# Optimization experiments

Measured on AMD Instinct MI355X. Metric: run time of the kernel, lower is better.

## Reference

```python
import jax, jax.numpy as jnp
import numpy as np

N_NODES = 8192
D_FEAT = 128
R_BITS = 8      # rows per band
B_BANDS = 64    # number of LSH bands
D_THRESH = 0.25 # cosine-distance threshold from LSH(z, d=0.25, ...)


def setup_inputs() -> dict:
    key = jax.random.key(0)
    k1, k2, k3 = jax.random.split(key, 3)
    z = jax.random.normal(k1, (N_NODES, D_FEAT), dtype=jnp.float32)
    # random hyperplanes for signed-projection LSH: r*b = 512 planes
    H = jax.random.normal(k2, (D_FEAT, R_BITS * B_BANDS), dtype=jnp.float32)
    edge_index = jax.random.randint(k3, (2, N_NODES * 16), 0, N_NODES, dtype=jnp.int64)
    return {"z": z, "H": H, "edge_index": edge_index}


def reference(z, H, edge_index):
    # edge_index is unused by forward_all (kept for signature fidelity).
    N = z.shape[0]
    # --- hyperplane LSH signatures ---
    bits = (z @ H) > 0                              # [N, r*b] bool
    bits = bits.reshape(N, B_BANDS, R_BITS)         # [N, b, r]
    powers = (2 ** jnp.arange(R_BITS)).astype(jnp.int32)
    codes = jnp.sum(bits.astype(jnp.int32) * powers, axis=-1)  # [N, b] band hash codes

    # --- candidate pairs: collide in at least one band (OR over bands) ---
    def band_or(mask, c):  # c: [N] codes for one band
        return mask | (c[:, None] == c[None, :]), None
    collide, _ = jax.lax.scan(band_or, jnp.zeros((N, N), dtype=bool), codes.T)

    # --- exact cosine similarity on candidates ---
    zn = z / jnp.linalg.norm(z, axis=1, keepdims=True)
    S = zn @ zn.T                                   # [N, N] cosine similarity
    dist = 1.0 - S                                  # cosine distance

    eye = jnp.eye(N, dtype=bool)
    # pairs kept by LSH: colliding, within distance threshold, off-diagonal
    keep = collide & (dist < D_THRESH) & (~eye)
    # adjacency[v1, v2] = 1 - dist = cos_sim (sigmoid=True path); identity on diagonal
    A = jnp.where(keep, S, 0.0) + eye.astype(S.dtype)
    return A
```

## Files before the change

kernel.cpp:

```cpp
#include <hip/hip_runtime.h>
#include <hip/hip_bf16.h>

#define N_NODES 8192
#define D_FEAT 128

typedef __bf16 bf16x8 __attribute__((ext_vector_type(8)));
typedef float f32x4 __attribute__((ext_vector_type(4)));

__device__ __forceinline__ void lgkm_barrier() {
  asm volatile("s_waitcnt lgkmcnt(0)\n\ts_barrier" ::: "memory");
}
__device__ __forceinline__ void lgkm_fence() {
  asm volatile("s_waitcnt lgkmcnt(0)" ::: "memory");
}

__device__ __attribute__((noinline)) bool lsh_collide(
    const float* __restrict__ z, const float* __restrict__ H, int i, int j) {
  for (int b = 0; b < 64; ++b) {
    unsigned ci = 0, cj = 0;
    for (int bit = 0; bit < 8; ++bit) {
      int col = b * 8 + bit;
      float di = 0.f, dj = 0.f;
      for (int k = 0; k < D_FEAT; ++k) {
        float h = H[(size_t)k * 512 + col];
        di += z[(size_t)i * D_FEAT + k] * h;
        dj += z[(size_t)j * D_FEAT + k] * h;
      }
      if (di > 0.f) ci |= (1u << bit);
      if (cj > 0.f) cj |= 0;
      if (dj > 0.f) cj |= (1u << bit);
    }
    if (ci == cj) return true;
  }
  return false;
}

__device__ __forceinline__ unsigned pack_bf16x2(float x, float y) {
  __hip_bfloat16 bx = __float2bfloat16(x), by = __float2bfloat16(y);
  return (unsigned)(*(unsigned short*)&bx) |
         ((unsigned)(*(unsigned short*)&by) << 16);
}

__device__ __forceinline__ void stage_tile128(const float* __restrict__ z, int blk,
                                              unsigned short (*T)[128], int tid) {
  int row = tid >> 1, half = tid & 1;
  const float4* src = (const float4*)(z + (size_t)(blk * 128 + row) * D_FEAT + half * 64);
  float4 v[16];
#pragma unroll
  for (int c = 0; c < 16; ++c) v[c] = src[c];
  float ss = 0.f;
#pragma unroll
  for (int c = 0; c < 16; ++c)
    ss += v[c].x * v[c].x + v[c].y * v[c].y + v[c].z * v[c].z + v[c].w * v[c].w;
  ss += __shfl_xor(ss, 1);
  float inv = rsqrtf(ss);
#pragma unroll
  for (int c = 0; c < 8; ++c) {
    float4 a = v[2 * c], b = v[2 * c + 1];
    uint4 o;
    o.x = pack_bf16x2(a.x * inv, a.y * inv);
    o.y = pack_bf16x2(a.z * inv, a.w * inv);
    o.z = pack_bf16x2(b.x * inv, b.y * inv);
    o.w = pack_bf16x2(b.z * inv, b.w * inv);
    ((uint4*)&T[row][0])[(half * 8 + c) ^ (row & 15)] = o;
  }
}

__device__ __forceinline__ void stage_tile64(const float* __restrict__ z, int row0,
                                             unsigned short (*T)[128], int tid) {
  int row = tid >> 2, q = tid & 3;
  const float4* src = (const float4*)(z + (size_t)(row0 + row) * D_FEAT + q * 32);
  float4 v[8];
#pragma unroll
  for (int c = 0; c < 8; ++c) v[c] = src[c];
  float ss = 0.f;
#pragma unroll
  for (int c = 0; c < 8; ++c)
    ss += v[c].x * v[c].x + v[c].y * v[c].y + v[c].z * v[c].z + v[c].w * v[c].w;
  ss += __shfl_xor(ss, 1);
  ss += __shfl_xor(ss, 2);
  float inv = rsqrtf(ss);
#pragma unroll
  for (int c = 0; c < 4; ++c) {
    float4 a = v[2 * c], b = v[2 * c + 1];
    uint4 o;
    o.x = pack_bf16x2(a.x * inv, a.y * inv);
    o.y = pack_bf16x2(a.z * inv, a.w * inv);
    o.z = pack_bf16x2(b.x * inv, b.y * inv);
    o.w = pack_bf16x2(b.z * inv, b.w * inv);
    ((uint4*)&T[row][0])[(q * 4 + c) ^ (row & 15)] = o;
  }
}

__global__ __launch_bounds__(256, 3) void sim_kernel(const float* __restrict__ z,
                                                     const float* __restrict__ H,
                                                     float* __restrict__ out) {
  __shared__ __align__(16) unsigned char smem_raw[49152];
  unsigned short (*As)[128] = (unsigned short (*)[128])smem_raw;
  unsigned short (*Bs)[128] = (unsigned short (*)[128])(smem_raw + 16384);
  float* fS = (float*)smem_raw;

  int tid = threadIdx.x;
  int b = (int)blockIdx.x;
  int bn = b & 63;
  int bm0 = b >> 6;

  int wv = tid >> 6, lane = tid & 63;
  int wm = (wv >> 1) * 32, wn = (wv & 1) * 64;
  int m16 = lane & 15, g = lane >> 4;
  float* slab = fS + wv * 1024;

  stage_tile128(z, bn, Bs, tid);

  for (int t = 0; t < 16; ++t) {
    int bm = bm0 * 16 + t;

    lgkm_barrier();
    stage_tile64(z, bm * 64, As, tid);
    lgkm_barrier();

    f32x4 acc[2][4] = {};
#pragma unroll
    for (int kc = 0; kc < 4; ++kc) {
      bf16x8 fa[2], fb[4];
      int chunk = kc * 4 + g;
      int cs = (chunk ^ m16) * 8;
#pragma unroll
      for (int tt = 0; tt < 2; ++tt) fa[tt] = *(const bf16x8*)&As[wm + tt * 16 + m16][cs];
#pragma unroll
      for (int tt = 0; tt < 4; ++tt) fb[tt] = *(const bf16x8*)&Bs[wn + tt * 16 + m16][cs];
#pragma unroll
      for (int tm = 0; tm < 2; ++tm)
#pragma unroll
        for (int tn = 0; tn < 4; ++tn)
          acc[tm][tn] = __builtin_amdgcn_mfma_f32_16x16x32_bf16(fa[tm], fb[tn], acc[tm][tn], 0, 0, 0);
    }

    lgkm_barrier();

#pragma unroll
    for (int tm = 0; tm < 2; ++tm) {
#pragma unroll
      for (int tn = 0; tn < 4; ++tn) {
        int colq = tn * 16 + m16;
        int j = bn * 128 + wn + colq;
        f32x4 c = acc[tm][tn];
#pragma unroll
        for (int r = 0; r < 4; ++r) {
          int rs = g * 4 + r;
          int i = bm * 64 + wm + tm * 16 + rs;
          float s = c[r];
          float val = 0.0f;
          if (i == j) {
            val = 1.0f;
          } else if (s > 0.75f) {
            if (lsh_collide(z, H, i, j)) val = s;
          }
          slab[rs * 64 + (((colq >> 2) ^ rs) << 2) + (colq & 3)] = val;
        }
      }
      lgkm_fence();
#pragma unroll
      for (int it = 0; it < 4; ++it) {
        int rs = it * 4 + g;
        f32x4 v = *(const f32x4*)&slab[rs * 64 + ((m16 ^ rs) << 2)];
        int grow = bm * 64 + wm + tm * 16 + rs;
        *(f32x4*)&out[(size_t)grow * N_NODES + bn * 128 + wn + m16 * 4] = v;
      }
    }
  }
}

extern "C" void kernel_launch(void* const* d_in, const int* in_sizes, int n_in,
                              void* d_out, int out_size, void* d_ws, size_t ws_size,
                              hipStream_t stream) {
  const float* z = (const float*)d_in[0];
  const float* H = (const float*)d_in[1];
  float* out = (float*)d_out;
  (void)d_ws; (void)ws_size;

  sim_kernel<<<512, 256, 0, stream>>>(z, H, out);
}
```

Measured before the change: 281.1 us.

## Add dedicated store warps to overlap output writes with next tile compute

The block grows to 512 threads. Four waves compute the MFMA tile and write the results into a 32 KB shared buffer, and four separate waves store the previous tile's results to global memory while the next tile is being staged and computed. This removes the compute waves' serialized epilogue stores and the per-wave slab barrier. In exchange it uses 80 KB of shared memory and twice as many threads per block, which lowers occupancy. The single shared output buffer depends on barrier ordering to avoid overwrite races.

New measurement: 476.3 us. 1.69x slower.

```diff
diff --git a/kernel.cpp b/kernel.cpp
--- a/kernel.cpp
+++ b/kernel.cpp
@@ -9,9 +9,6 @@
 
 __device__ __forceinline__ void lgkm_barrier() {
   asm volatile("s_waitcnt lgkmcnt(0)\n\ts_barrier" ::: "memory");
-}
-__device__ __forceinline__ void lgkm_fence() {
-  asm volatile("s_waitcnt lgkmcnt(0)" ::: "memory");
 }
 
 __device__ __attribute__((noinline)) bool lsh_collide(
@@ -27,7 +24,6 @@
         dj += z[(size_t)j * D_FEAT + k] * h;
       }
       if (di > 0.f) ci |= (1u << bit);
-      if (cj > 0.f) cj |= 0;
       if (dj > 0.f) cj |= (1u << bit);
     }
     if (ci == cj) return true;
@@ -92,83 +88,97 @@
   }
 }
 
-__global__ __launch_bounds__(256, 3) void sim_kernel(const float* __restrict__ z,
+__device__ __forceinline__ void store_fs(float* __restrict__ out,
+                                         const float* __restrict__ fS,
+                                         int bm, int bn, int st) {
+#pragma unroll
+  for (int it = 0; it < 8; ++it) {
+    int slot = st + 256 * it;
+    int row = slot >> 5, chunk = slot & 31;
+    f32x4 v = *(const f32x4*)&fS[row * 128 + ((chunk ^ (row & 31)) << 2)];
+    *(f32x4*)&out[(size_t)(bm * 64 + row) * N_NODES + bn * 128 + chunk * 4] = v;
+  }
+}
+
+__global__ __launch_bounds__(512, 4) void sim_kernel(const float* __restrict__ z,
                                                      const float* __restrict__ H,
                                                      float* __restrict__ out) {
-  __shared__ __align__(16) unsigned char smem_raw[49152];
+  __shared__ __align__(16) unsigned char smem_raw[81920];
   unsigned short (*As)[128] = (unsigned short (*)[128])smem_raw;
   unsigned short (*Bs)[128] = (unsigned short (*)[128])(smem_raw + 16384);
-  float* fS = (float*)smem_raw;
+  float* fS = (float*)(smem_raw + 49152);
 
   int tid = threadIdx.x;
   int b = (int)blockIdx.x;
   int bn = b & 63;
   int bm0 = b >> 6;
 
-  int wv = tid >> 6, lane = tid & 63;
-  int wm = (wv >> 1) * 32, wn = (wv & 1) * 64;
+  int wv = tid >> 6;
+  bool is_store = wv >= 4;
+  int st = tid & 255;
+
+  int cw = wv & 3, lane = tid & 63;
+  int wm = (cw >> 1) * 32, wn = (cw & 1) * 64;
   int m16 = lane & 15, g = lane >> 4;
-  float* slab = fS + wv * 1024;
 
-  stage_tile128(z, bn, Bs, tid);
+  if (!is_store) stage_tile128(z, bn, Bs, st);
 
   for (int t = 0; t < 16; ++t) {
     int bm = bm0 * 16 + t;
 
     lgkm_barrier();
-    stage_tile64(z, bm * 64, As, tid);
+    if (!is_store) {
+      stage_tile64(z, bm * 64, As, st);
+    } else if (t > 0) {
+      store_fs(out, fS, bm - 1, bn, st);
+    }
     lgkm_barrier();
 
-    f32x4 acc[2][4] = {};
+    if (!is_store) {
+      f32x4 acc[2][4] = {};
 #pragma unroll
-    for (int kc = 0; kc < 4; ++kc) {
-      bf16x8 fa[2], fb[4];
-      int chunk = kc * 4 + g;
-      int cs = (chunk ^ m16) * 8;
+      for (int kc = 0; kc < 4; ++kc) {
+        bf16x8 fa[2], fb[4];
+        int chunk = kc * 4 + g;
+        int cs = (chunk ^ m16) * 8;
 #pragma unroll
-      for (int tt = 0; tt < 2; ++tt) fa[tt] = *(const bf16x8*)&As[wm + tt * 16 + m16][cs];
+        for (int tt = 0; tt < 2; ++tt) fa[tt] = *(const bf16x8*)&As[wm + tt * 16 + m16][cs];
 #pragma unroll
-      for (int tt = 0; tt < 4; ++tt) fb[tt] = *(const bf16x8*)&Bs[wn + tt * 16 + m16][cs];
+        for (int tt = 0; tt < 4; ++tt) fb[tt] = *(const bf16x8*)&Bs[wn + tt * 16 + m16][cs];
 #pragma unroll
-      for (int tm = 0; tm < 2; ++tm)
+        for (int tm = 0; tm < 2; ++tm)
 #pragma unroll
-        for (int tn = 0; tn < 4; ++tn)
-          acc[tm][tn] = __builtin_amdgcn_mfma_f32_16x16x32_bf16(fa[tm], fb[tn], acc[tm][tn], 0, 0, 0);
-    }
-
-    lgkm_barrier();
+          for (int tn = 0; tn < 4; ++tn)
+            acc[tm][tn] = __builtin_amdgcn_mfma_f32_16x16x32_bf16(fa[tm], fb[tn], acc[tm][tn], 0, 0, 0);
+      }
 
 #pragma unroll
-    for (int tm = 0; tm < 2; ++tm) {
+      for (int tm = 0; tm < 2; ++tm) {
 #pragma unroll
-      for (int tn = 0; tn < 4; ++tn) {
-        int colq = tn * 16 + m16;
-        int j = bn * 128 + wn + colq;
-        f32x4 c = acc[tm][tn];
+        for (int tn = 0; tn < 4; ++tn) {
+          int col = wn + tn * 16 + m16;
+          int j = bn * 128 + col;
+          f32x4 c = acc[tm][tn];
 #pragma unroll
-        for (int r = 0; r < 4; ++r) {
-          int rs = g * 4 + r;
-          int i = bm * 64 + wm + tm * 16 + rs;
-          float s = c[r];
-          float val = 0.0f;
-          if (i == j) {
-            val = 1.0f;
-          } else if (s > 0.75f) {
-            if (lsh_collide(z, H, i, j)) val = s;
+          for (int r = 0; r < 4; ++r) {
+            int row = wm + tm * 16 + g * 4 + r;
+            int i = bm * 64 + row;
+            float s = c[r];
+            float val = 0.0f;
+            if (i == j) {
+              val = 1.0f;
+            } else if (s > 0.75f) {
+              if (lsh_collide(z, H, i, j)) val = s;
+            }
+            fS[row * 128 + ((((col >> 2) ^ (row & 31)) << 2) | (col & 3))] = val;
           }
-          slab[rs * 64 + (((colq >> 2) ^ rs) << 2) + (colq & 3)] = val;
         }
-      }
-      lgkm_fence();
-#pragma unroll
-      for (int it = 0; it < 4; ++it) {
-        int rs = it * 4 + g;
-        f32x4 v = *(const f32x4*)&slab[rs * 64 + ((m16 ^ rs) << 2)];
-        int grow = bm * 64 + wm + tm * 16 + rs;
-        *(f32x4*)&out[(size_t)grow * N_NODES + bn * 128 + wn + m16 * 4] = v;
       }
     }
   }
+
+  lgkm_barrier();
+  if (is_store) store_fs(out, fS, bm0 * 16 + 15, bn, st);
 }
 
 extern "C" void kernel_launch(void* const* d_in, const int* in_sizes, int n_in,
@@ -179,5 +189,5 @@
   float* out = (float*)d_out;
   (void)d_ws; (void)ws_size;
 
-  sim_kernel<<<512, 256, 0, stream>>>(z, H, out);
+  sim_kernel<<<512, 512, 0, stream>>>(z, H, out);
 }
```
